# Optimization experiments

Measured on AMD Instinct MI355X. Metric: run time of the kernel, lower is better.

## Reference

```python
import jax, jax.numpy as jnp
import numpy as np

BLOCK_L = 32
STRIDE = 16
DIM = 128
N_DOWN = 5  # log2(BLOCK_L)


def setup_inputs() -> dict:
    key = jax.random.key(0)
    ks = jax.random.split(key, 4)
    B, H, S, D = 2, 16, 8192, DIM
    k = jax.random.normal(ks[0], (B, H, S, D), dtype=jnp.float32)
    pe = jax.random.normal(ks[1], (BLOCK_L, D), dtype=jnp.float32)
    # torch Linear weights [out, in]; down: Linear(2*dim, dim), scaled like default init
    w_down = jax.random.normal(ks[2], (N_DOWN, D, 2 * D), dtype=jnp.float32) / jnp.sqrt(2.0 * D)
    w_stop = jax.random.normal(ks[3], (D, D), dtype=jnp.float32) / jnp.sqrt(1.0 * D)
    return {"k": k, "pe": pe, "w_down": w_down, "w_stop": w_stop}


def reference(k, pe, w_down, w_stop):
    B, H, S, D = k.shape
    L = pe.shape[0]
    nb = (S - L) // STRIDE + 1  # number of sliding windows
    # unfold(-2, L, STRIDE).mT -> [B, H, nb, L, D]
    idx = STRIDE * jnp.arange(nb)[:, None] + jnp.arange(L)[None, :]  # [nb, L]
    x = k[:, :, idx, :] + pe  # broadcast pe over [B, H, nb]
    # prepend a zero block along the window axis
    x = jnp.concatenate([jnp.zeros_like(x[:, :, :1]), x], axis=2)  # [B, H, nb+1, L, D]
    # Phi: hierarchical pairwise merge, log2(L) stages
    for i in range(N_DOWN):
        Lc = x.shape[-2]
        x = x.reshape(*x.shape[:-2], Lc // 2, 2 * D)
        x = jax.nn.silu(jnp.einsum('...i,oi->...o', x, w_down[i]))
    out = jnp.einsum('...i,oi->...o', x, w_stop)  # [B, H, nb+1, 1, D]
    return out.squeeze(-2)
```

## Files before the change

kernel.cpp:

```cpp
#include <hip/hip_runtime.h>

#define BQ 2
#define HQ 16
#define SQ 8192
#define DQ 128
#define STR 16
#define NWIN 511
#define NBLK 512
#define WPB 8
#define NWG_PER_HEAD 64

typedef float f32x4 __attribute__((ext_vector_type(4)));
typedef short s16x8 __attribute__((ext_vector_type(8)));
typedef short s16x4 __attribute__((ext_vector_type(4)));

#define R_KIN 0u
#define R_S0  20480u
#define R_S1  0u
#define R_S2  20480u
#define R_S3  0u
#define R_S4  28672u

static __device__ __forceinline__ unsigned swz(unsigned b) {
    return b ^ (((b >> 9) & 7u) << 4);
}

static __device__ __forceinline__ short f2bf(float f) {
    __bf16 h = (__bf16)f;
    return __builtin_bit_cast(short, h);
}

static __device__ __forceinline__ float silu(float v) {
    return v * __builtin_amdgcn_rcpf(1.f + __expf(-v));
}

__global__ void prep_kernel(const float* __restrict__ wd,
                            const float* __restrict__ wstop,
                            const float* __restrict__ pe,
                            short* __restrict__ o,
                            float* __restrict__ bias,
                            float* __restrict__ out) {
    int blk = blockIdx.x;
    if (blk < 704) {
        int i = blk * 256 + threadIdx.x;
        if (i < 163840) {
            int s   = i >> 15;
            int r   = i & 32767;
            int ct  = r >> 12;
            int r2  = r & 4095;
            int kt  = r2 >> 9;
            int r3  = r2 & 511;
            int ln  = r3 >> 3;
            int e   = r3 & 7;
            int ch  = ct * 16 + (ln & 15);
            int k   = kt * 32 + (ln >> 4) * 8 + e;
            o[i] = f2bf(wd[((size_t)(s * 128 + ch)) * 256 + k]);
        } else if (i < 180224) {
            int j   = i - 163840;
            int ct  = j >> 11;
            int r2  = j & 2047;
            int kt  = r2 >> 9;
            int r3  = r2 & 511;
            int ln  = r3 >> 3;
            int e   = r3 & 7;
            int ch  = ct * 16 + (ln & 15);
            int k   = kt * 32 + (ln >> 4) * 8 + e;
            o[i] = f2bf(wstop[ch * 128 + k]);
        }
    } else if (blk < 712) {
        int oo = (blk - 704) * 256 + threadIdx.x;
        int j = oo >> 7;
        int c = oo & 127;
        const float* w  = wd + (size_t)c * 256;
        const float* p0 = pe + (2 * j) * DQ;
        const float* p1 = pe + (2 * j + 1) * DQ;
        float s = 0.f;
        #pragma unroll 4
        for (int i = 0; i < 128; ++i) s += w[i] * p0[i];
        #pragma unroll 4
        for (int i = 0; i < 128; ++i) s += w[i + 128] * p1[i];
        bias[oo] = s;
    } else {
        int i = (blk - 712) * 256 + threadIdx.x;
        int bh = i >> 7, d = i & 127;
        out[(size_t)bh * NBLK * DQ + d] = 0.f;
    }
}

__global__ __launch_bounds__(512, 6)
void fused_kernel(const float* __restrict__ kin,
                  const short* __restrict__ wdb,
                  const float* __restrict__ bias0,
                  float* __restrict__ out) {
    __shared__ __align__(16) unsigned char lds[53248];

    const int bh = blockIdx.x >> 6;
    const int w0 = (blockIdx.x & 63) * WPB;
    const int tid  = threadIdx.x;
    const int lane = tid & 63;
    const int ct   = tid >> 6;
    const int kl   = lane >> 4;
    const int nl   = lane & 15;

    const float* kb = kin + (size_t)bh * SQ * DQ;
    const short* wbase = wdb + ct * 4096 + lane * 8;

#define LOAD_KIN(cbase) {                                                      \
        _Pragma("unroll")                                                      \
        for (int it = 0; it < 3; ++it) {                                       \
            int task = tid + it * 512;                                         \
            if (task < 1280) {                                                 \
                int rr = task >> 4;                                            \
                int c8 = task & 15;                                            \
                int srow = STR * w0 + (cbase) + rr;                            \
                if (srow > SQ - 1) srow = SQ - 1;                              \
                const float* kp = kb + (size_t)srow * DQ + c8 * 8;             \
                f32x4 a0 = *(const f32x4*)kp;                                  \
                f32x4 a1 = *(const f32x4*)(kp + 4);                            \
                s16x8 v;                                                       \
                v[0]=f2bf(a0[0]); v[1]=f2bf(a0[1]); v[2]=f2bf(a0[2]); v[3]=f2bf(a0[3]); \
                v[4]=f2bf(a1[0]); v[5]=f2bf(a1[1]); v[6]=f2bf(a1[2]); v[7]=f2bf(a1[3]); \
                *(s16x8*)(lds + swz(R_KIN + (unsigned)((rr << 8) + (c8 << 4)))) = v; \
            }                                                                  \
        } }

#define K_HALF4(W0, W1, W2, W3, P, Q, off, accv) {                             \
        s16x8 aa0 = *(const s16x8*)((P) + (off));                              \
        s16x8 aa1 = *(const s16x8*)((Q) + (off));                              \
        s16x8 aa2 = *(const s16x8*)((P) + (off) + 128);                        \
        s16x8 aa3 = *(const s16x8*)((Q) + (off) + 128);                        \
        accv = __builtin_amdgcn_mfma_f32_16x16x32_bf16(W0, aa0, accv, 0, 0, 0); \
        accv = __builtin_amdgcn_mfma_f32_16x16x32_bf16(W1, aa1, accv, 0, 0, 0); \
        accv = __builtin_amdgcn_mfma_f32_16x16x32_bf16(W2, aa2, accv, 0, 0, 0); \
        accv = __builtin_amdgcn_mfma_f32_16x16x32_bf16(W3, aa3, accv, 0, 0, 0); }

#define K_FULL(P, Q, off, accv)                                                \
        K_HALF4(wf[0], wf[1], wf[2], wf[3], P, Q, (off),       accv)           \
        K_HALF4(wf[4], wf[5], wf[6], wf[7], P, Q, (off) + 256, accv)

#define WRITE_ROW(region, d, accv) {                                           \
        s16x4 v;                                                               \
        v[0] = f2bf(silu((accv)[0])); v[1] = f2bf(silu((accv)[1]));            \
        v[2] = f2bf(silu((accv)[2])); v[3] = f2bf(silu((accv)[3]));            \
        *(s16x4*)(lds + swz((region) + ((unsigned)(d) << 8)                    \
                            + (unsigned)(ct * 32 + kl * 8))) = v; }

#define LOAD_WF(stage_off) {                                                   \
        _Pragma("unroll")                                                      \
        for (int kt = 0; kt < 8; ++kt)                                         \
            wf[kt] = *(const s16x8*)(wbase + (stage_off) + kt * 512); }

    s16x8 wf[8];
    LOAD_WF(0);
    const f32x4 bias = *(const f32x4*)(bias0 + nl * 128 + ct * 16 + kl * 4);

    LOAD_KIN(0);
    __syncthreads();

    unsigned pb0 = swz(R_KIN + ((unsigned)(2 * nl) << 8) + (unsigned)(kl << 4));
    const unsigned char* P0 = lds + pb0;
    const unsigned char* Q0 = lds + (pb0 ^ 64u);

    {
        f32x4 acc0 = bias, acc1 = bias, acc2 = bias, acc3 = bias;
        K_FULL(P0, Q0, 0,     acc0);
        K_FULL(P0, Q0, 4096,  acc1);
        K_FULL(P0, Q0, 8192,  acc2);
        K_FULL(P0, Q0, 12288, acc3);
        WRITE_ROW(R_S0, nl,      acc0);
        WRITE_ROW(R_S0, 16 + nl, acc1);
        WRITE_ROW(R_S0, 32 + nl, acc2);
        WRITE_ROW(R_S0, 48 + nl, acc3);
    }
    __syncthreads();

    LOAD_KIN(64);
    __syncthreads();

    {
        f32x4 acc0 = bias, acc1 = bias, acc2 = bias, acc3 = bias;
        K_FULL(P0, Q0, 0,     acc0);
        K_FULL(P0, Q0, 4096,  acc1);
        K_FULL(P0, Q0, 8192,  acc2);
        K_FULL(P0, Q0, 12288, acc3);
        LOAD_WF(32768);
        WRITE_ROW(R_S0, 64 + nl,  acc0);
        WRITE_ROW(R_S0, 80 + nl,  acc1);
        WRITE_ROW(R_S0, 96 + nl,  acc2);
        WRITE_ROW(R_S0, 112 + nl, acc3);
    }
    __syncthreads();

    {
        unsigned pb = swz(R_S0 + ((unsigned)(2 * nl) << 8) + (unsigned)(kl << 4));
        const unsigned char* P = lds + pb;
        const unsigned char* Q = lds + (pb ^ 64u);
        f32x4 acc0 = {}, acc1 = {}, acc2 = {}, acc3 = {};
        K_FULL(P, Q, 0,     acc0);
        K_FULL(P, Q, 8192,  acc1);
        K_FULL(P, Q, 16384, acc2);
        K_FULL(P, Q, 24576, acc3);
        LOAD_WF(2 * 32768);
        WRITE_ROW(R_S1, nl,      acc0);
        WRITE_ROW(R_S1, 16 + nl, acc1);
        WRITE_ROW(R_S1, 32 + nl, acc2);
        WRITE_ROW(R_S1, 48 + nl, acc3);
    }
    __syncthreads();

    {
        unsigned pb = swz(R_S1 + ((unsigned)(2 * nl) << 8) + (unsigned)(kl << 4));
        const unsigned char* P = lds + pb;
        const unsigned char* Q = lds + (pb ^ 64u);
        f32x4 acc0 = {}, acc1 = {};
        K_FULL(P, Q, 0,    acc0);
        K_FULL(P, Q, 8192, acc1);
        LOAD_WF(3 * 32768);
        WRITE_ROW(R_S2, nl,      acc0);
        WRITE_ROW(R_S2, 16 + nl, acc1);
    }
    __syncthreads();

    {
        unsigned pb = swz(R_S2 + ((unsigned)(2 * nl) << 8) + (unsigned)(kl << 4));
        const unsigned char* P = lds + pb;
        const unsigned char* Q = lds + (pb ^ 64u);
        f32x4 acc0 = {};
        K_FULL(P, Q, 0, acc0);
        LOAD_WF(4 * 32768);
        WRITE_ROW(R_S3, nl, acc0);
    }
    __syncthreads();

    {
        int dc = (nl < 8) ? nl : 7;
        unsigned pb = swz(R_S3 + ((unsigned)(2 * dc) << 8) + (unsigned)(kl << 4));
        const unsigned char* P = lds + pb;
        const unsigned char* Q = lds + (pb ^ 64u);
        f32x4 acc0 = {};
        K_FULL(P, Q, 0, acc0);
        #pragma unroll
        for (int kt = 0; kt < 4; ++kt)
            wf[kt] = *(const s16x8*)(wdb + 163840 + ct * 2048 + kt * 512 + lane * 8);
        if (nl < 8) WRITE_ROW(R_S4, nl, acc0);
    }
    __syncthreads();

    {
        int dc = (nl < 8) ? nl : 7;
        unsigned pb = swz(R_S4 + ((unsigned)dc << 8) + (unsigned)(kl << 4));
        const unsigned char* P = lds + pb;
        const unsigned char* Q = lds + (pb ^ 64u);
        f32x4 acc = {0.f, 0.f, 0.f, 0.f};
        K_HALF4(wf[0], wf[1], wf[2], wf[3], P, Q, 0, acc);
        int w = w0 + nl;
        if (nl < 8 && w < NWIN) {
            *(f32x4*)(out + ((size_t)bh * NBLK + (w + 1)) * DQ + ct * 16 + kl * 4) = acc;
        }
    }
#undef K_HALF4
#undef K_FULL
#undef WRITE_ROW
#undef LOAD_WF
#undef LOAD_KIN
}

extern "C" void kernel_launch(void* const* d_in, const int* in_sizes, int n_in,
                              void* d_out, int out_size, void* d_ws, size_t ws_size,
                              hipStream_t stream) {
    const float* kin   = (const float*)d_in[0];
    const float* pe    = (const float*)d_in[1];
    const float* wdown = (const float*)d_in[2];
    const float* wstop = (const float*)d_in[3];
    float* out = (float*)d_out;
    short* wbf  = (short*)d_ws;
    float* bias = (float*)((char*)d_ws + 360448);

    prep_kernel<<<728, 256, 0, stream>>>(wdown, wstop, pe, wbf, bias, out);
    fused_kernel<<<BQ * HQ * NWG_PER_HEAD, 512, 0, stream>>>(kin, wbf, bias, out);
}
```

Baseline: 76.55 us.

## Use 32x32x16 MFMA for first two merge stages with repacked weights

The first two down-projection stages switch from 16x16x32 bf16 MFMA to 32x32x16 bf16 MFMA. The prep kernel repacks the stage-0 and stage-1 weights into a 32-row tile layout, and new XOR-swizzle addressing is used for the LDS reads and writes. Weights for these stages are streamed from global memory per chunk instead of being held in registers. The goal is fewer MFMA instructions and less LDS operand traffic per output. The cost is more per-chunk global weight loads and a larger 16-wide accumulator that raises register pressure.

```diff
diff --git a/kernel.cpp b/kernel.cpp
--- a/kernel.cpp
+++ b/kernel.cpp
@@ -11,6 +11,7 @@
 #define NWG_PER_HEAD 64
 
 typedef float f32x4 __attribute__((ext_vector_type(4)));
+typedef float f32x16 __attribute__((ext_vector_type(16)));
 typedef short s16x8 __attribute__((ext_vector_type(8)));
 typedef short s16x4 __attribute__((ext_vector_type(4)));
 
@@ -43,9 +44,22 @@
     int blk = blockIdx.x;
     if (blk < 704) {
         int i = blk * 256 + threadIdx.x;
-        if (i < 163840) {
+        if (i < 65536) {
             int s   = i >> 15;
             int r   = i & 32767;
+            int ct  = r >> 13;
+            int r2  = r & 8191;
+            int t   = r2 >> 9;
+            int r3  = r2 & 511;
+            int ln  = r3 >> 3;
+            int e   = r3 & 7;
+            int ch  = ct * 32 + (ln & 31);
+            int k   = t * 16 + (ln >> 5) * 8 + e;
+            o[i] = f2bf(wd[((size_t)(s * 128 + ch)) * 256 + k]);
+        } else if (i < 163840) {
+            int j   = i - 65536;
+            int s   = j >> 15;
+            int r   = j & 32767;
             int ct  = r >> 12;
             int r2  = r & 4095;
             int kt  = r2 >> 9;
@@ -54,7 +68,7 @@
             int e   = r3 & 7;
             int ch  = ct * 16 + (ln & 15);
             int k   = kt * 32 + (ln >> 4) * 8 + e;
-            o[i] = f2bf(wd[((size_t)(s * 128 + ch)) * 256 + k]);
+            o[i] = f2bf(wd[((size_t)((s + 2) * 128 + ch)) * 256 + k]);
         } else if (i < 180224) {
             int j   = i - 163840;
             int ct  = j >> 11;
@@ -98,12 +112,16 @@
     const int w0 = (blockIdx.x & 63) * WPB;
     const int tid  = threadIdx.x;
     const int lane = tid & 63;
-    const int ct   = tid >> 6;
+    const int wave = tid >> 6;
     const int kl   = lane >> 4;
     const int nl   = lane & 15;
+    const int lo5  = lane & 31;
+    const int hi   = lane >> 5;
+    const int ct32 = wave & 3;
+    const int rg   = wave >> 2;
+    const int ct   = wave;
 
     const float* kb = kin + (size_t)bh * SQ * DQ;
-    const short* wbase = wdb + ct * 4096 + lane * 8;
 
 #define LOAD_KIN(cbase) {                                                      \
         _Pragma("unroll")                                                      \
@@ -124,6 +142,98 @@
             }                                                                  \
         } }
 
+    const unsigned kxr = ((unsigned)(lo5 & 7)) << 4;
+    const unsigned kxw = ((unsigned)((lo5 >> 1) & 7)) << 4;
+    const unsigned h4  = (((unsigned)hi) << 4) ^ kxr;
+    const unsigned rowb0 = R_KIN +
+        ((unsigned)(32 * rg + 16 * (lo5 >> 4) + 2 * (lo5 & 15)) << 8);
+
+#define S0_CHUNK(dbase) {                                                      \
+        f32x16 acc;                                                            \
+        _Pragma("unroll")                                                      \
+        for (int a = 0; a < 4; ++a) {                                          \
+            f32x4 b4 = *(const f32x4*)(bias0 + (lo5 & 15) * 128                \
+                                       + ct32 * 32 + a * 8 + hi * 4);          \
+            acc[4*a+0] = b4[0]; acc[4*a+1] = b4[1];                            \
+            acc[4*a+2] = b4[2]; acc[4*a+3] = b4[3];                            \
+        }                                                                      \
+        _Pragma("unroll")                                                      \
+        for (int c4 = 0; c4 < 4; ++c4) {                                       \
+            s16x8 wq[4];                                                       \
+            _Pragma("unroll")                                                  \
+            for (int q = 0; q < 4; ++q)                                        \
+                wq[q] = *(const s16x8*)(wdb + ct32 * 8192                      \
+                                        + (c4 * 4 + q) * 512 + lane * 8);      \
+            _Pragma("unroll")                                                  \
+            for (int q = 0; q < 4; ++q) {                                      \
+                const int t = c4 * 4 + q;                                      \
+                unsigned addr = rowb0 + ((t >= 8) ? 256u : 0u)                 \
+                              + (((unsigned)((t & 7) << 5)) ^ h4);             \
+                s16x8 bb = *(const s16x8*)(lds + addr);                        \
+                acc = __builtin_amdgcn_mfma_f32_32x32x16_bf16(wq[q], bb, acc, 0, 0, 0); \
+            }                                                                  \
+        }                                                                      \
+        const unsigned d = (unsigned)((dbase) + 32 * rg + lo5);                \
+        _Pragma("unroll")                                                      \
+        for (int a = 0; a < 4; ++a) {                                          \
+            s16x4 v;                                                           \
+            v[0] = f2bf(silu(acc[4*a+0])); v[1] = f2bf(silu(acc[4*a+1]));      \
+            v[2] = f2bf(silu(acc[4*a+2])); v[3] = f2bf(silu(acc[4*a+3]));      \
+            *(s16x4*)(lds + R_S0 + (d << 8)                                    \
+                      + (((unsigned)(ct32 * 64 + a * 16 + hi * 8)) ^ kxw)) = v;\
+        }                                                                      \
+    }
+
+    LOAD_KIN(0);
+    __syncthreads();
+
+    S0_CHUNK(0);
+    __syncthreads();
+
+    LOAD_KIN(64);
+    __syncthreads();
+
+    S0_CHUNK(64);
+    __syncthreads();
+
+    s16x8 wf[8];
+
+    {
+        const unsigned rowb1 = R_S0 + ((unsigned)(64 * rg + 2 * lo5) << 8);
+        f32x16 acc = {};
+        #pragma unroll
+        for (int c4 = 0; c4 < 4; ++c4) {
+            s16x8 wq[4];
+            #pragma unroll
+            for (int q = 0; q < 4; ++q)
+                wq[q] = *(const s16x8*)(wdb + 32768 + ct32 * 8192
+                                        + (c4 * 4 + q) * 512 + lane * 8);
+            #pragma unroll
+            for (int q = 0; q < 4; ++q) {
+                const int t = c4 * 4 + q;
+                unsigned addr = rowb1 + ((t >= 8) ? 256u : 0u)
+                              + (((unsigned)((t & 7) << 5)) ^ h4);
+                s16x8 bb = *(const s16x8*)(lds + addr);
+                acc = __builtin_amdgcn_mfma_f32_32x32x16_bf16(wq[q], bb, acc, 0, 0, 0);
+            }
+        }
+        #pragma unroll
+        for (int kt = 0; kt < 8; ++kt)
+            wf[kt] = *(const s16x8*)(wdb + 2 * 32768 + ct * 4096 + kt * 512 + lane * 8);
+        const unsigned d = (unsigned)(32 * rg + lo5);
+        #pragma unroll
+        for (int a = 0; a < 4; ++a) {
+            s16x4 v;
+            v[0] = f2bf(silu(acc[4*a+0])); v[1] = f2bf(silu(acc[4*a+1]));
+            v[2] = f2bf(silu(acc[4*a+2])); v[3] = f2bf(silu(acc[4*a+3]));
+            *(s16x4*)(lds + R_S1 + (d << 8)
+                      + (((unsigned)(ct32 * 64 + a * 16 + hi * 8)) ^ kxw)) = v;
+        }
+    }
+    __syncthreads();
+
+    const short* wbase = wdb + ct * 4096 + lane * 8;
+
 #define K_HALF4(W0, W1, W2, W3, P, Q, off, accv) {                             \
         s16x8 aa0 = *(const s16x8*)((P) + (off));                              \
         s16x8 aa1 = *(const s16x8*)((Q) + (off));                              \
@@ -149,64 +259,6 @@
         _Pragma("unroll")                                                      \
         for (int kt = 0; kt < 8; ++kt)                                         \
             wf[kt] = *(const s16x8*)(wbase + (stage_off) + kt * 512); }
-
-    s16x8 wf[8];
-    LOAD_WF(0);
-    const f32x4 bias = *(const f32x4*)(bias0 + nl * 128 + ct * 16 + kl * 4);
-
-    LOAD_KIN(0);
-    __syncthreads();
-
-    unsigned pb0 = swz(R_KIN + ((unsigned)(2 * nl) << 8) + (unsigned)(kl << 4));
-    const unsigned char* P0 = lds + pb0;
-    const unsigned char* Q0 = lds + (pb0 ^ 64u);
-
-    {
-        f32x4 acc0 = bias, acc1 = bias, acc2 = bias, acc3 = bias;
-        K_FULL(P0, Q0, 0,     acc0);
-        K_FULL(P0, Q0, 4096,  acc1);
-        K_FULL(P0, Q0, 8192,  acc2);
-        K_FULL(P0, Q0, 12288, acc3);
-        WRITE_ROW(R_S0, nl,      acc0);
-        WRITE_ROW(R_S0, 16 + nl, acc1);
-        WRITE_ROW(R_S0, 32 + nl, acc2);
-        WRITE_ROW(R_S0, 48 + nl, acc3);
-    }
-    __syncthreads();
-
-    LOAD_KIN(64);
-    __syncthreads();
-
-    {
-        f32x4 acc0 = bias, acc1 = bias, acc2 = bias, acc3 = bias;
-        K_FULL(P0, Q0, 0,     acc0);
-        K_FULL(P0, Q0, 4096,  acc1);
-        K_FULL(P0, Q0, 8192,  acc2);
-        K_FULL(P0, Q0, 12288, acc3);
-        LOAD_WF(32768);
-        WRITE_ROW(R_S0, 64 + nl,  acc0);
-        WRITE_ROW(R_S0, 80 + nl,  acc1);
-        WRITE_ROW(R_S0, 96 + nl,  acc2);
-        WRITE_ROW(R_S0, 112 + nl, acc3);
-    }
-    __syncthreads();
-
-    {
-        unsigned pb = swz(R_S0 + ((unsigned)(2 * nl) << 8) + (unsigned)(kl << 4));
-        const unsigned char* P = lds + pb;
-        const unsigned char* Q = lds + (pb ^ 64u);
-        f32x4 acc0 = {}, acc1 = {}, acc2 = {}, acc3 = {};
-        K_FULL(P, Q, 0,     acc0);
-        K_FULL(P, Q, 8192,  acc1);
-        K_FULL(P, Q, 16384, acc2);
-        K_FULL(P, Q, 24576, acc3);
-        LOAD_WF(2 * 32768);
-        WRITE_ROW(R_S1, nl,      acc0);
-        WRITE_ROW(R_S1, 16 + nl, acc1);
-        WRITE_ROW(R_S1, 32 + nl, acc2);
-        WRITE_ROW(R_S1, 48 + nl, acc3);
-    }
-    __syncthreads();
 
     {
         unsigned pb = swz(R_S1 + ((unsigned)(2 * nl) << 8) + (unsigned)(kl << 4));
@@ -263,6 +315,7 @@
 #undef WRITE_ROW
 #undef LOAD_WF
 #undef LOAD_KIN
+#undef S0_CHUNK
 }
 
 extern "C" void kernel_launch(void* const* d_in, const int* in_sizes, int n_in,
```

Result: slower. 88.42 us (+15.5%).
